# Performance work log

Measured on AMD Instinct MI355X. Metric: run time of the kernel, lower is better.

The kernel has to match this reference:

```python
import jax, jax.numpy as jnp
import numpy as np

B, LQ, LK, D, H = 4, 2048, 2048, 1024, 16
HD = D // H  # head dim = 64


def setup_inputs() -> dict:
    key = jax.random.key(0)
    ks = jax.random.split(key, 8)
    s = 1.0 / np.sqrt(D)
    return {
        "zt": jax.random.normal(ks[0], (B, LQ, D), jnp.float32),
        "ic": jax.random.normal(ks[1], (B, LK, D), jnp.float32),
        "Wq": jax.random.normal(ks[2], (D, D), jnp.float32) * s,
        "bq": jax.random.normal(ks[3], (D,), jnp.float32) * 0.01,
        "Wk": jax.random.normal(ks[4], (D, D), jnp.float32) * s,
        "bk": jax.random.normal(ks[5], (D,), jnp.float32) * 0.01,
        "Wv": jax.random.normal(ks[6], (D, D), jnp.float32) * s,
        "bv": jax.random.normal(ks[7], (D,), jnp.float32) * 0.01,
    }


def reference(zt, ic, Wq, bq, Wk, bk, Wv, bv):
    # Linear projections (torch Linear: x @ W.T + b); weights here stored as [out, in]
    q = zt @ Wq.T + bq            # [B, LQ, D]
    k = ic @ Wk.T + bk            # [B, LK, D]
    v = ic @ Wv.T + bv            # [B, LK, D]
    # split heads -> [B, H, L, HD]
    q = q.reshape(B, LQ, H, HD).transpose(0, 2, 1, 3)
    k = k.reshape(B, LK, H, HD).transpose(0, 2, 1, 3)
    v = v.reshape(B, LK, H, HD).transpose(0, 2, 1, 3)
    scale = 1.0 / jnp.sqrt(jnp.asarray(HD, q.dtype))
    scores = jnp.einsum('bhqd,bhkd->bhqk', q, k) * scale  # [B, H, LQ, LK]
    attn = jax.nn.softmax(scores, axis=-1)
    out = jnp.einsum('bhqk,bhkd->bhqd', attn, v)          # [B, H, LQ, HD]
    return out.transpose(0, 2, 1, 3).reshape(B, LQ, D)
```

## Files before the change

kernel.cpp:

```cpp
#include <hip/hip_runtime.h>
#include <hip/hip_bf16.h>
#include <cstdint>

#define B_  4
#define LQ_ 2048
#define LK_ 2048
#define D_  1024
#define H_  16
#define HD_ 64

typedef __attribute__((ext_vector_type(8))) short bf16x8;
typedef __attribute__((ext_vector_type(4))) float f32x4;

#if defined(__has_builtin)
#if __has_builtin(__builtin_amdgcn_exp2f)
#define EXP2F(x) __builtin_amdgcn_exp2f(x)
#else
#define EXP2F(x) exp2f(x)
#endif
#else
#define EXP2F(x) exp2f(x)
#endif

__device__ __forceinline__ unsigned short f2b(float f) {
    union { float f; unsigned u; } v; v.f = f;
    unsigned u = v.u;
    unsigned r = (u + 0x7fffu + ((u >> 16) & 1u)) >> 16;
    return (unsigned short)r;
}

__device__ __forceinline__ void gl_lds16(const unsigned short* g, unsigned short* l) {
    __builtin_amdgcn_global_load_lds(
        (const __attribute__((address_space(1))) unsigned int*)(g),
        (__attribute__((address_space(3))) unsigned int*)(l),
        16, 0, 0);
}

#define PHASE_BARRIER() do { \
    __builtin_amdgcn_sched_barrier(0); \
    __builtin_amdgcn_s_barrier(); \
    __builtin_amdgcn_sched_barrier(0); } while (0)

#define WAITVM(N) do { \
    asm volatile("s_waitcnt vmcnt(" #N ")" ::: "memory"); \
    __builtin_amdgcn_sched_barrier(0); } while (0)

__global__ void cvt_all(const float* __restrict__ a0, unsigned short* __restrict__ d0,
                        const float* __restrict__ a1, unsigned short* __restrict__ d1,
                        const float* __restrict__ w0, unsigned short* __restrict__ e0, float s0,
                        const float* __restrict__ w1, unsigned short* __restrict__ e1,
                        const float* __restrict__ w2, unsigned short* __restrict__ e2,
                        int nact, int nw) {
    const float* in; unsigned short* out; float s = 1.0f; int n;
    switch (blockIdx.y) {
        case 0: in = a0; out = d0; n = nact; break;
        case 1: in = a1; out = d1; n = nact; break;
        case 2: in = w0; out = e0; n = nw; s = s0; break;
        case 3: in = w1; out = e1; n = nw; break;
        default: in = w2; out = e2; n = nw; break;
    }
    int i = (blockIdx.x * blockDim.x + threadIdx.x) * 8;
    int stride = gridDim.x * blockDim.x * 8;
    for (; i < n; i += stride) {
        float4 x = *(const float4*)(in + i);
        float4 y = *(const float4*)(in + i + 4);
        bf16x8 v;
        v[0] = (short)f2b(x.x * s); v[1] = (short)f2b(x.y * s);
        v[2] = (short)f2b(x.z * s); v[3] = (short)f2b(x.w * s);
        v[4] = (short)f2b(y.x * s); v[5] = (short)f2b(y.y * s);
        v[6] = (short)f2b(y.z * s); v[7] = (short)f2b(y.w * s);
        *(bf16x8*)(out + i) = v;
    }
}

__global__ __launch_bounds__(512, 2) void qkv_gemm(
    const unsigned short* __restrict__ Xq,
    const unsigned short* __restrict__ Xkv,
    const unsigned short* __restrict__ Wqb, const unsigned short* __restrict__ Wkb,
    const unsigned short* __restrict__ Wvb,
    const float* __restrict__ bq, const float* __restrict__ bk,
    const float* __restrict__ bv, float qscale,
    unsigned short* __restrict__ Qb, unsigned short* __restrict__ Kb,
    unsigned short* __restrict__ Vb)
{
    __shared__ unsigned short AS[4][8192];
    __shared__ unsigned short BS[4][8192];

    const int proj = blockIdx.y >> 2;
    const int nt0  = blockIdx.y & 3;
    const unsigned short* X = (proj == 0) ? Xq : Xkv;
    const unsigned short* W = (proj == 0) ? Wqb : (proj == 1 ? Wkb : Wvb);
    const float* bias       = (proj == 0) ? bq  : (proj == 1 ? bk  : bv);
    unsigned short* Y       = (proj == 0) ? Qb  : (proj == 1 ? Kb  : Vb);
    const float bscale      = (proj == 0) ? qscale : 1.0f;

    const int tid  = threadIdx.x;
    const int lane = tid & 63;
    const int w    = tid >> 6;
    const int wm   = w & 1, wn = w >> 1;
    const int m0   = blockIdx.x * 256;
    const int n0   = nt0 * 256;
    const int l15  = lane & 15, quad = lane >> 4;

    f32x4 acc[8][4] = {};

    const unsigned short* gA0 = X + (size_t)(m0 + (w * 2) * 16 + l15) * 1024 + quad * 8;
    const unsigned short* gA1 = gA0 + 16 * 1024;
    const unsigned short* gB0 = W + (size_t)(n0 + (w * 2) * 16 + l15) * 1024 + quad * 8;
    const unsigned short* gB1 = gB0 + 16 * 1024;

#define STAGE_A(slot, koff) do { \
    gl_lds16(gA0 + (koff), &AS[slot][(w * 2) * 512 + lane * 8]); \
    gl_lds16(gA1 + (koff), &AS[slot][(w * 2 + 1) * 512 + lane * 8]); } while (0)
#define STAGE_B(slot, koff) do { \
    gl_lds16(gB0 + (koff), &BS[slot][(w * 2) * 512 + lane * 8]); \
    gl_lds16(gB1 + (koff), &BS[slot][(w * 2 + 1) * 512 + lane * 8]); } while (0)

    const int aoff = (wm * 8) * 512 + lane * 8;
    const int boff = (wn * 4) * 512 + lane * 8;

    STAGE_A(0, 0);   STAGE_B(0, 0);
    STAGE_A(1, 32);  STAGE_B(1, 32);
    STAGE_A(2, 64);  STAGE_B(2, 64);
    WAITVM(8);
    __builtin_amdgcn_s_barrier();
    __builtin_amdgcn_sched_barrier(0);

    #pragma unroll 2
    for (int t = 0; t < 16; ++t) {
        const int s0 = (2 * t) & 3;
        const int s1 = (2 * t + 1) & 3;
        const int s3 = (2 * t + 3) & 3;

        bf16x8 af[8], bf0, bf1;

        #pragma unroll
        for (int i = 0; i < 8; ++i)
            af[i] = *(const bf16x8*)(&AS[s0][aoff + i * 512]);
        bf0 = *(const bf16x8*)(&BS[s0][boff]);
        bf1 = *(const bf16x8*)(&BS[s0][boff + 512]);
        PHASE_BARRIER();
        __builtin_amdgcn_s_setprio(1);
        #pragma unroll
        for (int i = 0; i < 8; ++i) {
            acc[i][0] = __builtin_amdgcn_mfma_f32_16x16x32_bf16(af[i], bf0, acc[i][0], 0, 0, 0);
            acc[i][1] = __builtin_amdgcn_mfma_f32_16x16x32_bf16(af[i], bf1, acc[i][1], 0, 0, 0);
        }
        __builtin_amdgcn_s_setprio(0);
        if (t < 15) STAGE_A(s3, (t + 1) * 64 + 32);

        bf0 = *(const bf16x8*)(&BS[s0][boff + 1024]);
        bf1 = *(const bf16x8*)(&BS[s0][boff + 1536]);
        if (t < 14) { WAITVM(6); } else { WAITVM(0); }
        PHASE_BARRIER();
        __builtin_amdgcn_s_setprio(1);
        #pragma unroll
        for (int i = 0; i < 8; ++i) {
            acc[i][2] = __builtin_amdgcn_mfma_f32_16x16x32_bf16(af[i], bf0, acc[i][2], 0, 0, 0);
            acc[i][3] = __builtin_amdgcn_mfma_f32_16x16x32_bf16(af[i], bf1, acc[i][3], 0, 0, 0);
        }
        __builtin_amdgcn_s_setprio(0);
        if (t < 15) STAGE_B(s3, (t + 1) * 64 + 32);

        #pragma unroll
        for (int i = 0; i < 8; ++i)
            af[i] = *(const bf16x8*)(&AS[s1][aoff + i * 512]);
        bf0 = *(const bf16x8*)(&BS[s1][boff]);
        bf1 = *(const bf16x8*)(&BS[s1][boff + 512]);
        PHASE_BARRIER();
        __builtin_amdgcn_s_setprio(1);
        #pragma unroll
        for (int i = 0; i < 8; ++i) {
            acc[i][0] = __builtin_amdgcn_mfma_f32_16x16x32_bf16(af[i], bf0, acc[i][0], 0, 0, 0);
            acc[i][1] = __builtin_amdgcn_mfma_f32_16x16x32_bf16(af[i], bf1, acc[i][1], 0, 0, 0);
        }
        __builtin_amdgcn_s_setprio(0);
        if (t < 14) STAGE_A(s0, (t + 2) * 64);

        bf0 = *(const bf16x8*)(&BS[s1][boff + 1024]);
        bf1 = *(const bf16x8*)(&BS[s1][boff + 1536]);
        if (t < 14) { WAITVM(6); } else if (t == 14) { WAITVM(4); }
        PHASE_BARRIER();
        __builtin_amdgcn_s_setprio(1);
        #pragma unroll
        for (int i = 0; i < 8; ++i) {
            acc[i][2] = __builtin_amdgcn_mfma_f32_16x16x32_bf16(af[i], bf0, acc[i][2], 0, 0, 0);
            acc[i][3] = __builtin_amdgcn_mfma_f32_16x16x32_bf16(af[i], bf1, acc[i][3], 0, 0, 0);
        }
        __builtin_amdgcn_s_setprio(0);
        if (t < 14) STAGE_B(s0, (t + 2) * 64);
    }

#undef STAGE_A
#undef STAGE_B

    float bvv[4];
    #pragma unroll
    for (int j = 0; j < 4; ++j)
        bvv[j] = bias[n0 + wn * 64 + j * 16 + l15] * bscale;

    #pragma unroll
    for (int i = 0; i < 8; ++i) {
        #pragma unroll
        for (int r = 0; r < 4; ++r) {
            int row = m0 + wm * 128 + i * 16 + quad * 4 + r;
            unsigned short* yp = Y + (size_t)row * 1024 + n0 + wn * 64;
            #pragma unroll
            for (int j = 0; j < 4; ++j)
                yp[j * 16 + l15] = f2b(acc[i][j][r] + bvv[j]);
        }
    }
}

__global__ __launch_bounds__(256) void transpose_v(
    const unsigned short* __restrict__ Vb, unsigned short* __restrict__ Vt)
{
    __shared__ unsigned short L[64 * 72];
    const int t0 = blockIdx.x * 64, h = blockIdx.y, b = blockIdx.z;
    const int rr = threadIdx.x >> 3;
    const int cc = (threadIdx.x & 7) * 8;

    #pragma unroll
    for (int p = 0; p < 2; ++p) {
        int r = rr + p * 32;
        *(bf16x8*)(&L[r * 72 + cc]) =
            *(const bf16x8*)(Vb + (size_t)(b * 2048 + t0 + r) * 1024 + h * 64 + cc);
    }
    __syncthreads();
    #pragma unroll
    for (int p = 0; p < 2; ++p) {
        int d = rr + p * 32;
        bf16x8 v;
        #pragma unroll
        for (int j = 0; j < 8; ++j)
            v[j] = (short)L[(cc + j) * 72 + d];
        *(bf16x8*)(Vt + ((size_t)(b * 16 + h) * 64 + d) * 2048 + t0 + cc) = v;
    }
}

__global__ __launch_bounds__(256, 2) void attn_kernel(
    const unsigned short* __restrict__ Q,
    const unsigned short* __restrict__ Kp,
    const unsigned short* __restrict__ Vt,
    float* __restrict__ Out)
{
    __shared__ unsigned short Ks[16 * 512];
    __shared__ unsigned short Vs[16 * 512];
    __shared__ unsigned short Ps[4][4096];

    const int tid  = threadIdx.x;
    const int lane = tid & 63;
    const int w    = tid >> 6;
    const int l15  = lane & 15, quad = lane >> 4;
    const int b = blockIdx.z, h = blockIdx.y, qt = blockIdx.x;

    bf16x8 qf[4][2];
    #pragma unroll
    for (int half = 0; half < 4; ++half) {
        const unsigned short* qptr =
            Q + (size_t)(b * LQ_ + qt * 256 + w * 64 + half * 16 + l15) * 1024 + h * 64;
        qf[half][0] = *(const bf16x8*)(qptr + quad * 8);
        qf[half][1] = *(const bf16x8*)(qptr + 32 + quad * 8);
    }

    bf16x8 ones;
    #pragma unroll
    for (int j = 0; j < 8; ++j) ones[j] = (short)0x3F80;

    f32x4 oacc[4][4] = {};
    f32x4 lacc[4]    = {};

    const unsigned short* Kbase = Kp + (size_t)b * LK_ * 1024 + h * 64;
    const unsigned short* Vbase = Vt + (size_t)(b * 16 + h) * 64 * 2048;

    const unsigned short* gK[4];
    unsigned short* lK[4];
    const unsigned short* gV[4];
    unsigned short* lV[4];
    #pragma unroll
    for (int j = 0; j < 4; ++j) {
        int kt = w + (j >> 1) * 4, dblk = j & 1;
        gK[j] = Kbase + (size_t)(kt * 16 + l15) * 1024 + dblk * 32 + quad * 8;
        lK[j] = &Ks[(kt * 2 + dblk) * 512 + lane * 8];
        gV[j] = Vbase + (size_t)(w * 16 + l15) * 2048 + j * 32 + quad * 8;
        lV[j] = &Vs[(w * 4 + j) * 512 + lane * 8];
    }

    const int pws = (quad >> 1) * 128 + l15 * 8 + (quad & 1) * 4;
    unsigned short* PwB = &Ps[w][pws];
    const unsigned short* PrB = &Ps[w][lane * 8];
    const unsigned short* Kfr = &Ks[lane * 8];
    const unsigned short* Vfr = &Vs[lane * 8];

    for (int k0 = 0; k0 < LK_; k0 += 128) {
        __syncthreads();
        #pragma unroll
        for (int j = 0; j < 4; ++j) {
            gl_lds16(gK[j] + (size_t)k0 * 1024, lK[j]);
            gl_lds16(gV[j] + k0, lV[j]);
        }
        __syncthreads();

        #pragma unroll
        for (int cc = 0; cc < 2; ++cc) {
            f32x4 st[4][4] = {};
            #pragma unroll
            for (int t = 0; t < 4; ++t)
                #pragma unroll
                for (int dblk = 0; dblk < 2; ++dblk) {
                    bf16x8 kf = *(const bf16x8*)(Kfr + ((cc * 4 + t) * 2 + dblk) * 512);
                    #pragma unroll
                    for (int half = 0; half < 4; ++half)
                        st[half][t] = __builtin_amdgcn_mfma_f32_16x16x32_bf16(
                            kf, qf[half][dblk], st[half][t], 0, 0, 0);
                }

            #pragma unroll
            for (int half = 0; half < 4; ++half) {
                unsigned short* pw = PwB + half * 1024;
                #pragma unroll
                for (int t = 0; t < 4; ++t) {
                    unsigned u0 = __float_as_uint(EXP2F(st[half][t][0])) + 0x8000u;
                    unsigned u1 = __float_as_uint(EXP2F(st[half][t][1])) + 0x8000u;
                    unsigned u2 = __float_as_uint(EXP2F(st[half][t][2])) + 0x8000u;
                    unsigned u3 = __float_as_uint(EXP2F(st[half][t][3])) + 0x8000u;
                    uint2 pk;
                    pk.x = __builtin_amdgcn_perm(u1, u0, 0x07060302);
                    pk.y = __builtin_amdgcn_perm(u3, u2, 0x07060302);
                    *(uint2*)(pw + t * 256) = pk;
                }
            }

            #pragma unroll
            for (int hbl = 0; hbl < 2; ++hbl) {
                bf16x8 pf[4];
                #pragma unroll
                for (int half = 0; half < 4; ++half) {
                    pf[half] = *(const bf16x8*)(PrB + half * 1024 + hbl * 512);
                    lacc[half] = __builtin_amdgcn_mfma_f32_16x16x32_bf16(
                        pf[half], ones, lacc[half], 0, 0, 0);
                }
                int hb = cc * 2 + hbl;
                #pragma unroll
                for (int nt = 0; nt < 4; ++nt) {
                    bf16x8 vf = *(const bf16x8*)(Vfr + (nt * 4 + hb) * 512);
                    #pragma unroll
                    for (int half = 0; half < 4; ++half)
                        oacc[half][nt] = __builtin_amdgcn_mfma_f32_16x16x32_bf16(
                            pf[half], vf, oacc[half][nt], 0, 0, 0);
                }
            }
        }
    }

    #pragma unroll
    for (int half = 0; half < 4; ++half) {
        float il[4];
        #pragma unroll
        for (int r = 0; r < 4; ++r) il[r] = 1.0f / lacc[half][r];
        #pragma unroll
        for (int nt = 0; nt < 4; ++nt) {
            #pragma unroll
            for (int r = 0; r < 4; ++r) {
                size_t orow = (size_t)(b * LQ_ + qt * 256 + w * 64 + half * 16 + quad * 4 + r);
                Out[orow * 1024 + h * 64 + nt * 16 + l15] = oacc[half][nt][r] * il[r];
            }
        }
    }
}

extern "C" void kernel_launch(void* const* d_in, const int* in_sizes, int n_in,
                              void* d_out, int out_size, void* d_ws, size_t ws_size,
                              hipStream_t stream) {
    const float* zt = (const float*)d_in[0];
    const float* ic = (const float*)d_in[1];
    const float* Wq = (const float*)d_in[2];
    const float* bq = (const float*)d_in[3];
    const float* Wk = (const float*)d_in[4];
    const float* bk = (const float*)d_in[5];
    const float* Wv = (const float*)d_in[6];
    const float* bv = (const float*)d_in[7];
    float* out = (float*)d_out;

    const size_t M8 = (size_t)8192 * 1024;
    const size_t M1 = (size_t)1024 * 1024;
    unsigned short* Qb  = (unsigned short*)d_ws;
    unsigned short* Kb  = Qb  + M8;
    unsigned short* Vb  = Kb  + M8;
    unsigned short* Xz  = Vb  + M8;
    unsigned short* Xi  = Xz  + M8;
    unsigned short* Wqb = Xi  + M8;
    unsigned short* Wkb = Wqb + M1;
    unsigned short* Wvb = Wkb + M1;
    unsigned short* Vtb = Xz;

    const float qscale = 0.125f * 1.44269504088896f;

    dim3 gcv(4096, 5);
    cvt_all<<<gcv, 256, 0, stream>>>(zt, Xz, ic, Xi,
                                     Wq, Wqb, qscale, Wk, Wkb, Wv, Wvb,
                                     (int)M8, (int)M1);

    dim3 gproj(32, 12);
    qkv_gemm<<<gproj, 512, 0, stream>>>(Xz, Xi, Wqb, Wkb, Wvb,
                                        bq, bk, bv, qscale, Qb, Kb, Vb);

    dim3 gtr(32, 16, 4);
    transpose_v<<<gtr, 256, 0, stream>>>(Vb, Vtb);

    dim3 gattn(8, 16, 4);
    attn_kernel<<<gattn, 256, 0, stream>>>(Qb, Kb, Vtb, out);
}
```

Before: 304.4 us.

## Double-buffer K tiles in LDS, load V directly to registers, remap block order

```diff
diff --git a/kernel.cpp b/kernel.cpp
--- a/kernel.cpp
+++ b/kernel.cpp
@@ -244,15 +244,21 @@
     const unsigned short* __restrict__ Vt,
     float* __restrict__ Out)
 {
-    __shared__ unsigned short Ks[16 * 512];
-    __shared__ unsigned short Vs[16 * 512];
+    __shared__ unsigned short Ks[2][16 * 512];
     __shared__ unsigned short Ps[4][4096];
 
     const int tid  = threadIdx.x;
     const int lane = tid & 63;
     const int w    = tid >> 6;
     const int l15  = lane & 15, quad = lane >> 4;
-    const int b = blockIdx.z, h = blockIdx.y, qt = blockIdx.x;
+
+    const int bid = blockIdx.x + (blockIdx.y << 3) + (blockIdx.z << 7);
+    const int glo = bid & 7;
+    const int jx  = bid >> 3;
+    const int qt  = jx & 7;
+    const int g   = glo + ((jx >> 3) << 3);
+    const int h   = g & 15;
+    const int b   = g >> 4;
 
     bf16x8 qf[4][2];
     #pragma unroll
@@ -275,59 +281,70 @@
 
     const unsigned short* gK[4];
     unsigned short* lK[4];
-    const unsigned short* gV[4];
-    unsigned short* lV[4];
     #pragma unroll
     for (int j = 0; j < 4; ++j) {
         int kt = w + (j >> 1) * 4, dblk = j & 1;
         gK[j] = Kbase + (size_t)(kt * 16 + l15) * 1024 + dblk * 32 + quad * 8;
-        lK[j] = &Ks[(kt * 2 + dblk) * 512 + lane * 8];
-        gV[j] = Vbase + (size_t)(w * 16 + l15) * 2048 + j * 32 + quad * 8;
-        lV[j] = &Vs[(w * 4 + j) * 512 + lane * 8];
+        lK[j] = &Ks[0][(kt * 2 + dblk) * 512 + lane * 8];
     }
 
     const int pws = (quad >> 1) * 128 + l15 * 8 + (quad & 1) * 4;
     unsigned short* PwB = &Ps[w][pws];
     const unsigned short* PrB = &Ps[w][lane * 8];
-    const unsigned short* Kfr = &Ks[lane * 8];
-    const unsigned short* Vfr = &Vs[lane * 8];
-
-    for (int k0 = 0; k0 < LK_; k0 += 128) {
-        __syncthreads();
-        #pragma unroll
-        for (int j = 0; j < 4; ++j) {
-            gl_lds16(gK[j] + (size_t)k0 * 1024, lK[j]);
-            gl_lds16(gV[j] + k0, lV[j]);
-        }
-        __syncthreads();
+    const unsigned short* KfrB = &Ks[0][lane * 8];
+    const unsigned short* Vg = Vbase + (size_t)l15 * 2048 + quad * 8;
+
+    #pragma unroll
+    for (int j = 0; j < 4; ++j) gl_lds16(gK[j], lK[j]);
+    WAITVM(0);
+    PHASE_BARRIER();
+
+    for (int t = 0; t < 16; ++t) {
+        const int cur = t & 1;
+        if (t < 15) {
+            const int stoff = (cur ^ 1) * 8192;
+            #pragma unroll
+            for (int j = 0; j < 4; ++j)
+                gl_lds16(gK[j] + (size_t)(t + 1) * (128 * 1024), lK[j] + stoff);
+        }
+        const unsigned short* Kfr = KfrB + cur * 8192;
+        const int k0 = t * 128;
 
         #pragma unroll
         for (int cc = 0; cc < 2; ++cc) {
+            bf16x8 vreg[2][4];
+            #pragma unroll
+            for (int hbl = 0; hbl < 2; ++hbl)
+                #pragma unroll
+                for (int nt = 0; nt < 4; ++nt)
+                    vreg[hbl][nt] = *(const bf16x8*)(
+                        Vg + (size_t)nt * 32768 + k0 + (cc * 2 + hbl) * 32);
+
             f32x4 st[4][4] = {};
             #pragma unroll
-            for (int t = 0; t < 4; ++t)
+            for (int ti = 0; ti < 4; ++ti)
                 #pragma unroll
                 for (int dblk = 0; dblk < 2; ++dblk) {
-                    bf16x8 kf = *(const bf16x8*)(Kfr + ((cc * 4 + t) * 2 + dblk) * 512);
+                    bf16x8 kf = *(const bf16x8*)(Kfr + ((cc * 4 + ti) * 2 + dblk) * 512);
                     #pragma unroll
                     for (int half = 0; half < 4; ++half)
-                        st[half][t] = __builtin_amdgcn_mfma_f32_16x16x32_bf16(
-                            kf, qf[half][dblk], st[half][t], 0, 0, 0);
+                        st[half][ti] = __builtin_amdgcn_mfma_f32_16x16x32_bf16(
+                            kf, qf[half][dblk], st[half][ti], 0, 0, 0);
                 }
 
             #pragma unroll
             for (int half = 0; half < 4; ++half) {
                 unsigned short* pw = PwB + half * 1024;
                 #pragma unroll
-                for (int t = 0; t < 4; ++t) {
-                    unsigned u0 = __float_as_uint(EXP2F(st[half][t][0])) + 0x8000u;
-                    unsigned u1 = __float_as_uint(EXP2F(st[half][t][1])) + 0x8000u;
-                    unsigned u2 = __float_as_uint(EXP2F(st[half][t][2])) + 0x8000u;
-                    unsigned u3 = __float_as_uint(EXP2F(st[half][t][3])) + 0x8000u;
+                for (int ti = 0; ti < 4; ++ti) {
+                    unsigned u0 = __float_as_uint(EXP2F(st[half][ti][0])) + 0x8000u;
+                    unsigned u1 = __float_as_uint(EXP2F(st[half][ti][1])) + 0x8000u;
+                    unsigned u2 = __float_as_uint(EXP2F(st[half][ti][2])) + 0x8000u;
+                    unsigned u3 = __float_as_uint(EXP2F(st[half][ti][3])) + 0x8000u;
                     uint2 pk;
                     pk.x = __builtin_amdgcn_perm(u1, u0, 0x07060302);
                     pk.y = __builtin_amdgcn_perm(u3, u2, 0x07060302);
-                    *(uint2*)(pw + t * 256) = pk;
+                    *(uint2*)(pw + ti * 256) = pk;
                 }
             }
 
@@ -340,16 +357,19 @@
                     lacc[half] = __builtin_amdgcn_mfma_f32_16x16x32_bf16(
                         pf[half], ones, lacc[half], 0, 0, 0);
                 }
-                int hb = cc * 2 + hbl;
                 #pragma unroll
                 for (int nt = 0; nt < 4; ++nt) {
-                    bf16x8 vf = *(const bf16x8*)(Vfr + (nt * 4 + hb) * 512);
                     #pragma unroll
                     for (int half = 0; half < 4; ++half)
                         oacc[half][nt] = __builtin_amdgcn_mfma_f32_16x16x32_bf16(
-                            pf[half], vf, oacc[half][nt], 0, 0, 0);
+                            pf[half], vreg[hbl][nt], oacc[half][nt], 0, 0, 0);
                 }
             }
+        }
+
+        if (t < 15) {
+            WAITVM(0);
+            PHASE_BARRIER();
         }
     }
 
```

Measured after the change: 315.3 us. +3.6%, slower.
